# Kernel tuning notes

Hardware: AMD Instinct MI355X
Metric: run time of the kernel (lower is better)

The kernel has to match this reference:

```python
import jax, jax.numpy as jnp
import numpy as np

N_USERS = 50000
N_ITEMS = 50000
N_NODES = N_USERS + N_ITEMS   # 100000
EMB_DIM = 128
N_LAYERS = 3
N_EDGES = 600000


def _segment_softmax(logits, seg, num_segments):
    # numerically-stable softmax over edges grouped by segment id
    m = jax.ops.segment_max(logits, seg, num_segments=num_segments)
    e = jnp.exp(logits - m[seg])
    s = jax.ops.segment_sum(e, seg, num_segments=num_segments)
    return e / s[seg]


def setup_inputs() -> dict:
    key = jax.random.key(0)
    k1, k2, k3, k4 = jax.random.split(key, 4)
    embedding = jax.random.normal(k1, (N_NODES, EMB_DIM), jnp.float32) * 0.1  # init std=0.1
    src = jax.random.randint(k2, (N_EDGES,), 0, N_NODES, dtype=jnp.int32)
    tgt = jax.random.randint(k3, (N_EDGES,), 0, N_NODES, dtype=jnp.int32)
    edge_index = jnp.stack([src, tgt], axis=0)  # [2, E]
    edge_attrs = jax.random.normal(k4, (N_EDGES,), jnp.float32)
    return {"embedding": embedding, "edge_index": edge_index, "edge_attrs": edge_attrs}


def reference(embedding, edge_index, edge_attrs):
    from_, to_ = edge_index[0], edge_index[1]
    # DySimGCF edge normalization: sqrt(incoming_softmax * outgoing_softmax)
    incoming = _segment_softmax(edge_attrs, to_, N_NODES)
    outgoing = _segment_softmax(edge_attrs, from_, N_NODES)
    norm = jnp.sqrt(incoming * outgoing)  # [E]

    emb0 = embedding
    embs = [emb0]
    emb = emb0
    for _ in range(N_LAYERS):
        # gather source embeddings, scale, scatter-add into targets
        msgs = norm[:, None] * emb[from_]                         # [E, D]
        emb = jax.ops.segment_sum(msgs, to_, num_segments=N_NODES)  # [N, D]
        embs.append(emb)
    out = jnp.mean(jnp.stack(embs, axis=0), axis=0)  # layer-averaged embeddings
    return (emb0, out)
```

## Files before the change

### kernel.cpp

```cpp
#include <hip/hip_runtime.h>
#include <math.h>

#define N_NODES 100000
#define EMB_DIM 128
#define N_EDGES 600000
#define SCAN_BLOCKS ((N_NODES + 255) / 256)

__global__ void k_init(float* __restrict__ sum_out, int* __restrict__ deg) {
    int i = blockIdx.x * blockDim.x + threadIdx.x;
    if (i < N_NODES) {
        sum_out[i] = 0.0f;
        deg[i]     = 0;
    }
}

__global__ void k_edge(const int* __restrict__ from_, const int* __restrict__ to_,
                       const float* __restrict__ attr,
                       float* __restrict__ sum_out, int* __restrict__ deg) {
    int e = blockIdx.x * blockDim.x + threadIdx.x;
    if (e >= N_EDGES) return;
    atomicAdd(&sum_out[from_[e]], expf(attr[e]));
    atomicAdd(&deg[to_[e]], 1);
}

__global__ void k_scan1(const int* __restrict__ deg, int* __restrict__ local,
                        int* __restrict__ blockSums) {
    __shared__ int tmp[256];
    int t = threadIdx.x;
    int i = blockIdx.x * 256 + t;
    int v = (i < N_NODES) ? deg[i] : 0;
    tmp[t] = v;
    __syncthreads();
    for (int ofs = 1; ofs < 256; ofs <<= 1) {
        int add = (t >= ofs) ? tmp[t - ofs] : 0;
        __syncthreads();
        tmp[t] += add;
        __syncthreads();
    }
    if (i < N_NODES) local[i] = tmp[t] - v;
    if (t == 255) blockSums[blockIdx.x] = tmp[255];
}

__global__ void k_scan2(int* __restrict__ blockSums) {
    __shared__ int tmp[256];
    int t = threadIdx.x;
    int i0 = t * 2, i1 = t * 2 + 1;
    int a = (i0 < SCAN_BLOCKS) ? blockSums[i0] : 0;
    int b = (i1 < SCAN_BLOCKS) ? blockSums[i1] : 0;
    int s = a + b;
    tmp[t] = s;
    __syncthreads();
    for (int ofs = 1; ofs < 256; ofs <<= 1) {
        int add = (t >= ofs) ? tmp[t - ofs] : 0;
        __syncthreads();
        tmp[t] += add;
        __syncthreads();
    }
    int pre = tmp[t] - s;
    if (i0 < SCAN_BLOCKS) blockSums[i0] = pre;
    if (i1 < SCAN_BLOCKS) blockSums[i1] = pre + a;
}

__global__ void k_scan3(const int* __restrict__ local, const int* __restrict__ blockSums,
                        int* __restrict__ row_ptr, int* __restrict__ cursor) {
    int i = blockIdx.x * 256 + threadIdx.x;
    if (i < N_NODES) {
        int r = local[i] + blockSums[blockIdx.x];
        row_ptr[i] = r;
        cursor[i]  = r;
    }
    if (i == 0) row_ptr[N_NODES] = N_EDGES;
}

__global__ void k_fill(const int* __restrict__ from_, const int* __restrict__ to_,
                       const float* __restrict__ attr,
                       int* __restrict__ cursor, int* __restrict__ col,
                       float* __restrict__ val) {
    int e = blockIdx.x * blockDim.x + threadIdx.x;
    if (e >= N_EDGES) return;
    int t = to_[e];
    int pos = atomicAdd(&cursor[t], 1);
    col[pos] = from_[e];
    val[pos] = expf(attr[e]);
}

__global__ void k_norm(const int* __restrict__ row_ptr, const int* __restrict__ col,
                       const float* __restrict__ sum_out, float* __restrict__ val) {
    int r = blockIdx.x * 256 + threadIdx.x;
    if (r >= N_NODES) return;
    int beg = row_ptr[r], end = row_ptr[r + 1];
    float s = 0.0f;
    for (int e = beg; e < end; ++e) s += val[e];
    for (int e = beg; e < end; ++e) {
        val[e] = val[e] * rsqrtf(s * sum_out[col[e]]);
    }
}

template<int MODE>
__launch_bounds__(256)
__global__ void k_spmm(const int* __restrict__ row_ptr, const int* __restrict__ col,
                       const float* __restrict__ val,
                       const float* __restrict__ src, float* __restrict__ dst,
                       float* __restrict__ acc, const float* __restrict__ emb0) {
    int gid = blockIdx.x * 256 + threadIdx.x;
    int row = gid >> 4;
    if (row >= N_NODES) return;
    int lane = threadIdx.x & 15;
    int beg = row_ptr[row], end = row_ptr[row + 1];
    int d0 = lane * 4;
    float4 s0 = make_float4(0.f, 0.f, 0.f, 0.f);
    float4 s1 = make_float4(0.f, 0.f, 0.f, 0.f);
    int e = beg;
    for (; e + 2 <= end; e += 2) {
        int   c0 = col[e],   c1 = col[e + 1];
        float v0 = val[e],   v1 = val[e + 1];
        const float* b0 = src + (size_t)c0 * EMB_DIM + d0;
        const float* b1 = src + (size_t)c1 * EMB_DIM + d0;
        float4 x0 = *reinterpret_cast<const float4*>(b0);
        float4 x1 = *reinterpret_cast<const float4*>(b0 + 64);
        float4 y0 = *reinterpret_cast<const float4*>(b1);
        float4 y1 = *reinterpret_cast<const float4*>(b1 + 64);
        s0.x = fmaf(v0, x0.x, s0.x); s0.y = fmaf(v0, x0.y, s0.y);
        s0.z = fmaf(v0, x0.z, s0.z); s0.w = fmaf(v0, x0.w, s0.w);
        s1.x = fmaf(v0, x1.x, s1.x); s1.y = fmaf(v0, x1.y, s1.y);
        s1.z = fmaf(v0, x1.z, s1.z); s1.w = fmaf(v0, x1.w, s1.w);
        s0.x = fmaf(v1, y0.x, s0.x); s0.y = fmaf(v1, y0.y, s0.y);
        s0.z = fmaf(v1, y0.z, s0.z); s0.w = fmaf(v1, y0.w, s0.w);
        s1.x = fmaf(v1, y1.x, s1.x); s1.y = fmaf(v1, y1.y, s1.y);
        s1.z = fmaf(v1, y1.z, s1.z); s1.w = fmaf(v1, y1.w, s1.w);
    }
    if (e < end) {
        int   c = col[e];
        float v = val[e];
        const float* base = src + (size_t)c * EMB_DIM + d0;
        float4 x0 = *reinterpret_cast<const float4*>(base);
        float4 x1 = *reinterpret_cast<const float4*>(base + 64);
        s0.x = fmaf(v, x0.x, s0.x); s0.y = fmaf(v, x0.y, s0.y);
        s0.z = fmaf(v, x0.z, s0.z); s0.w = fmaf(v, x0.w, s0.w);
        s1.x = fmaf(v, x1.x, s1.x); s1.y = fmaf(v, x1.y, s1.y);
        s1.z = fmaf(v, x1.z, s1.z); s1.w = fmaf(v, x1.w, s1.w);
    }
    size_t o = (size_t)row * EMB_DIM + d0;
    if (MODE != 2) {
        *reinterpret_cast<float4*>(dst + o)      = s0;
        *reinterpret_cast<float4*>(dst + o + 64) = s1;
    }
    float4 a0, a1;
    if (MODE == 0) {
        float4 z0 = *reinterpret_cast<const float4*>(emb0 + o);
        float4 z1 = *reinterpret_cast<const float4*>(emb0 + o + 64);
        a0.x = z0.x + s0.x; a0.y = z0.y + s0.y; a0.z = z0.z + s0.z; a0.w = z0.w + s0.w;
        a1.x = z1.x + s1.x; a1.y = z1.y + s1.y; a1.z = z1.z + s1.z; a1.w = z1.w + s1.w;
    } else {
        a0 = *reinterpret_cast<float4*>(acc + o);
        a1 = *reinterpret_cast<float4*>(acc + o + 64);
        a0.x += s0.x; a0.y += s0.y; a0.z += s0.z; a0.w += s0.w;
        a1.x += s1.x; a1.y += s1.y; a1.z += s1.z; a1.w += s1.w;
        if (MODE == 2) {
            a0.x *= 0.25f; a0.y *= 0.25f; a0.z *= 0.25f; a0.w *= 0.25f;
            a1.x *= 0.25f; a1.y *= 0.25f; a1.z *= 0.25f; a1.w *= 0.25f;
        }
    }
    *reinterpret_cast<float4*>(acc + o)      = a0;
    *reinterpret_cast<float4*>(acc + o + 64) = a1;
}

extern "C" void kernel_launch(void* const* d_in, const int* in_sizes, int n_in,
                              void* d_out, int out_size, void* d_ws, size_t ws_size,
                              hipStream_t stream) {
    const float* embedding  = (const float*)d_in[0];
    const int*   edge_index = (const int*)d_in[1];
    const float* edge_attrs = (const float*)d_in[2];
    const int* from_ = edge_index;
    const int* to_   = edge_index + N_EDGES;

    float* out_emb0 = (float*)d_out;
    float* acc      = (float*)d_out + (size_t)N_NODES * EMB_DIM;
    float* buf1     = out_emb0;

    char* ws = (char*)d_ws;
    size_t off = 0;
    auto alloc = [&](size_t bytes) -> void* {
        void* p = ws + off;
        off += (bytes + 255) & ~(size_t)255;
        return p;
    };
    float* buf0    = (float*)alloc(sizeof(float) * (size_t)N_NODES * EMB_DIM);
    float* sum_out = (float*)alloc(sizeof(float) * N_NODES);
    int*   deg     = (int*)  alloc(sizeof(int)   * N_NODES);
    int*   scanloc = (int*)  alloc(sizeof(int)   * N_NODES);
    int*   bsums   = (int*)  alloc(sizeof(int)   * SCAN_BLOCKS);
    int*   row_ptr = (int*)  alloc(sizeof(int)   * (N_NODES + 1));
    int*   cursor  = (int*)  alloc(sizeof(int)   * N_NODES);
    int*   col     = (int*)  alloc(sizeof(int)   * N_EDGES);
    float* val     = (float*)alloc(sizeof(float) * N_EDGES);

    const int nblk = SCAN_BLOCKS;
    const int eblk = (N_EDGES + 255) / 256;
    const int sblk = (N_NODES * 16 + 255) / 256;

    k_init<<<nblk, 256, 0, stream>>>(sum_out, deg);
    k_edge<<<eblk, 256, 0, stream>>>(from_, to_, edge_attrs, sum_out, deg);
    k_scan1<<<nblk, 256, 0, stream>>>(deg, scanloc, bsums);
    k_scan2<<<1, 256, 0, stream>>>(bsums);
    k_scan3<<<nblk, 256, 0, stream>>>(scanloc, bsums, row_ptr, cursor);
    k_fill<<<eblk, 256, 0, stream>>>(from_, to_, edge_attrs, cursor, col, val);
    k_norm<<<nblk, 256, 0, stream>>>(row_ptr, col, sum_out, val);

    k_spmm<0><<<sblk, 256, 0, stream>>>(row_ptr, col, val, embedding, buf0, acc, embedding);
    k_spmm<1><<<sblk, 256, 0, stream>>>(row_ptr, col, val, buf0, buf1, acc, embedding);
    k_spmm<2><<<sblk, 256, 0, stream>>>(row_ptr, col, val, buf1, buf0, acc, embedding);

    hipMemcpyAsync(out_emb0, embedding, sizeof(float) * (size_t)N_NODES * EMB_DIM,
                   hipMemcpyDeviceToDevice, stream);
}
```

Baseline: 425.2 us.

## Store intermediate layer embeddings in bf16 and fuse final layer averaging

Converts the input embedding to packed bf16 and keeps the intermediate layer outputs in bf16, which halves the bytes read by each gather-heavy SpMM. The final layer kernel now computes the layer mean in one place from emb0, the two bf16 intermediates and its own result, and it also writes the emb0 copy, so the running accumulator and the separate memcpy are gone. The edge loop is unrolled to 4 edges. The trade-off is bf16 rounding error accumulating across layers, which may break a tight tolerance.

```diff
diff --git a/kernel.cpp b/kernel.cpp
--- a/kernel.cpp
+++ b/kernel.cpp
@@ -1,10 +1,16 @@
 #include <hip/hip_runtime.h>
 #include <math.h>
+#include <stdint.h>
 
 #define N_NODES 100000
 #define EMB_DIM 128
 #define N_EDGES 600000
 #define SCAN_BLOCKS ((N_NODES + 255) / 256)
+
+__device__ __forceinline__ unsigned int f2b(float f) {
+    unsigned int b = __float_as_uint(f);
+    return (b + 0x7FFFu + ((b >> 16) & 1u)) >> 16;
+}
 
 __global__ void k_init(float* __restrict__ sum_out, int* __restrict__ deg) {
     int i = blockIdx.x * blockDim.x + threadIdx.x;
@@ -96,73 +102,90 @@
     }
 }
 
-template<int MODE>
+__global__ void k_cvt(const float* __restrict__ in, uint4* __restrict__ out) {
+    int i = blockIdx.x * 256 + threadIdx.x;
+    const int total = N_NODES * EMB_DIM / 8;
+    if (i >= total) return;
+    const float4* p = reinterpret_cast<const float4*>(in) + (size_t)i * 2;
+    float4 a = p[0], b = p[1];
+    uint4 q;
+    q.x = f2b(a.x) | (f2b(a.y) << 16);
+    q.y = f2b(a.z) | (f2b(a.w) << 16);
+    q.z = f2b(b.x) | (f2b(b.y) << 16);
+    q.w = f2b(b.z) | (f2b(b.w) << 16);
+    out[i] = q;
+}
+
+#define UNPACK_FMA(q, v)                                      \
+    s0 = fmaf(v, __uint_as_float((q).x << 16), s0);           \
+    s1 = fmaf(v, __uint_as_float((q).x & 0xFFFF0000u), s1);   \
+    s2 = fmaf(v, __uint_as_float((q).y << 16), s2);           \
+    s3 = fmaf(v, __uint_as_float((q).y & 0xFFFF0000u), s3);   \
+    s4 = fmaf(v, __uint_as_float((q).z << 16), s4);           \
+    s5 = fmaf(v, __uint_as_float((q).z & 0xFFFF0000u), s5);   \
+    s6 = fmaf(v, __uint_as_float((q).w << 16), s6);           \
+    s7 = fmaf(v, __uint_as_float((q).w & 0xFFFF0000u), s7);
+
+template<int FINAL>
 __launch_bounds__(256)
 __global__ void k_spmm(const int* __restrict__ row_ptr, const int* __restrict__ col,
                        const float* __restrict__ val,
-                       const float* __restrict__ src, float* __restrict__ dst,
-                       float* __restrict__ acc, const float* __restrict__ emb0) {
+                       const uint4* __restrict__ srcb, uint4* __restrict__ dstb,
+                       const float* __restrict__ emb0,
+                       const uint4* __restrict__ e1b, const uint4* __restrict__ e2b,
+                       float* __restrict__ out_acc, float* __restrict__ out_emb0) {
     int gid = blockIdx.x * 256 + threadIdx.x;
     int row = gid >> 4;
     if (row >= N_NODES) return;
     int lane = threadIdx.x & 15;
     int beg = row_ptr[row], end = row_ptr[row + 1];
-    int d0 = lane * 4;
-    float4 s0 = make_float4(0.f, 0.f, 0.f, 0.f);
-    float4 s1 = make_float4(0.f, 0.f, 0.f, 0.f);
+    float s0 = 0.f, s1 = 0.f, s2 = 0.f, s3 = 0.f, s4 = 0.f, s5 = 0.f, s6 = 0.f, s7 = 0.f;
     int e = beg;
-    for (; e + 2 <= end; e += 2) {
-        int   c0 = col[e],   c1 = col[e + 1];
-        float v0 = val[e],   v1 = val[e + 1];
-        const float* b0 = src + (size_t)c0 * EMB_DIM + d0;
-        const float* b1 = src + (size_t)c1 * EMB_DIM + d0;
-        float4 x0 = *reinterpret_cast<const float4*>(b0);
-        float4 x1 = *reinterpret_cast<const float4*>(b0 + 64);
-        float4 y0 = *reinterpret_cast<const float4*>(b1);
-        float4 y1 = *reinterpret_cast<const float4*>(b1 + 64);
-        s0.x = fmaf(v0, x0.x, s0.x); s0.y = fmaf(v0, x0.y, s0.y);
-        s0.z = fmaf(v0, x0.z, s0.z); s0.w = fmaf(v0, x0.w, s0.w);
-        s1.x = fmaf(v0, x1.x, s1.x); s1.y = fmaf(v0, x1.y, s1.y);
-        s1.z = fmaf(v0, x1.z, s1.z); s1.w = fmaf(v0, x1.w, s1.w);
-        s0.x = fmaf(v1, y0.x, s0.x); s0.y = fmaf(v1, y0.y, s0.y);
-        s0.z = fmaf(v1, y0.z, s0.z); s0.w = fmaf(v1, y0.w, s0.w);
-        s1.x = fmaf(v1, y1.x, s1.x); s1.y = fmaf(v1, y1.y, s1.y);
-        s1.z = fmaf(v1, y1.z, s1.z); s1.w = fmaf(v1, y1.w, s1.w);
-    }
-    if (e < end) {
+    for (; e + 4 <= end; e += 4) {
+        int   c0 = col[e], c1 = col[e + 1], c2 = col[e + 2], c3 = col[e + 3];
+        float v0 = val[e], v1 = val[e + 1], v2 = val[e + 2], v3 = val[e + 3];
+        uint4 qa = srcb[(size_t)c0 * 16 + lane];
+        uint4 qb = srcb[(size_t)c1 * 16 + lane];
+        uint4 qc = srcb[(size_t)c2 * 16 + lane];
+        uint4 qd = srcb[(size_t)c3 * 16 + lane];
+        UNPACK_FMA(qa, v0)
+        UNPACK_FMA(qb, v1)
+        UNPACK_FMA(qc, v2)
+        UNPACK_FMA(qd, v3)
+    }
+    for (; e < end; ++e) {
         int   c = col[e];
         float v = val[e];
-        const float* base = src + (size_t)c * EMB_DIM + d0;
-        float4 x0 = *reinterpret_cast<const float4*>(base);
-        float4 x1 = *reinterpret_cast<const float4*>(base + 64);
-        s0.x = fmaf(v, x0.x, s0.x); s0.y = fmaf(v, x0.y, s0.y);
-        s0.z = fmaf(v, x0.z, s0.z); s0.w = fmaf(v, x0.w, s0.w);
-        s1.x = fmaf(v, x1.x, s1.x); s1.y = fmaf(v, x1.y, s1.y);
-        s1.z = fmaf(v, x1.z, s1.z); s1.w = fmaf(v, x1.w, s1.w);
-    }
-    size_t o = (size_t)row * EMB_DIM + d0;
-    if (MODE != 2) {
-        *reinterpret_cast<float4*>(dst + o)      = s0;
-        *reinterpret_cast<float4*>(dst + o + 64) = s1;
-    }
-    float4 a0, a1;
-    if (MODE == 0) {
-        float4 z0 = *reinterpret_cast<const float4*>(emb0 + o);
-        float4 z1 = *reinterpret_cast<const float4*>(emb0 + o + 64);
-        a0.x = z0.x + s0.x; a0.y = z0.y + s0.y; a0.z = z0.z + s0.z; a0.w = z0.w + s0.w;
-        a1.x = z1.x + s1.x; a1.y = z1.y + s1.y; a1.z = z1.z + s1.z; a1.w = z1.w + s1.w;
+        uint4 q = srcb[(size_t)c * 16 + lane];
+        UNPACK_FMA(q, v)
+    }
+    if (!FINAL) {
+        uint4 q;
+        q.x = f2b(s0) | (f2b(s1) << 16);
+        q.y = f2b(s2) | (f2b(s3) << 16);
+        q.z = f2b(s4) | (f2b(s5) << 16);
+        q.w = f2b(s6) | (f2b(s7) << 16);
+        dstb[(size_t)row * 16 + lane] = q;
     } else {
-        a0 = *reinterpret_cast<float4*>(acc + o);
-        a1 = *reinterpret_cast<float4*>(acc + o + 64);
-        a0.x += s0.x; a0.y += s0.y; a0.z += s0.z; a0.w += s0.w;
-        a1.x += s1.x; a1.y += s1.y; a1.z += s1.z; a1.w += s1.w;
-        if (MODE == 2) {
-            a0.x *= 0.25f; a0.y *= 0.25f; a0.z *= 0.25f; a0.w *= 0.25f;
-            a1.x *= 0.25f; a1.y *= 0.25f; a1.z *= 0.25f; a1.w *= 0.25f;
-        }
-    }
-    *reinterpret_cast<float4*>(acc + o)      = a0;
-    *reinterpret_cast<float4*>(acc + o + 64) = a1;
+        size_t o = (size_t)row * EMB_DIM + lane * 8;
+        float4 a0 = *reinterpret_cast<const float4*>(emb0 + o);
+        float4 a1 = *reinterpret_cast<const float4*>(emb0 + o + 4);
+        *reinterpret_cast<float4*>(out_emb0 + o)     = a0;
+        *reinterpret_cast<float4*>(out_emb0 + o + 4) = a1;
+        uint4 q1 = e1b[(size_t)row * 16 + lane];
+        uint4 q2 = e2b[(size_t)row * 16 + lane];
+        float4 r0, r1;
+        r0.x = (a0.x + __uint_as_float(q1.x << 16)          + __uint_as_float(q2.x << 16)          + s0) * 0.25f;
+        r0.y = (a0.y + __uint_as_float(q1.x & 0xFFFF0000u)  + __uint_as_float(q2.x & 0xFFFF0000u)  + s1) * 0.25f;
+        r0.z = (a0.z + __uint_as_float(q1.y << 16)          + __uint_as_float(q2.y << 16)          + s2) * 0.25f;
+        r0.w = (a0.w + __uint_as_float(q1.y & 0xFFFF0000u)  + __uint_as_float(q2.y & 0xFFFF0000u)  + s3) * 0.25f;
+        r1.x = (a1.x + __uint_as_float(q1.z << 16)          + __uint_as_float(q2.z << 16)          + s4) * 0.25f;
+        r1.y = (a1.y + __uint_as_float(q1.z & 0xFFFF0000u)  + __uint_as_float(q2.z & 0xFFFF0000u)  + s5) * 0.25f;
+        r1.z = (a1.z + __uint_as_float(q1.w << 16)          + __uint_as_float(q2.w << 16)          + s6) * 0.25f;
+        r1.w = (a1.w + __uint_as_float(q1.w & 0xFFFF0000u)  + __uint_as_float(q2.w & 0xFFFF0000u)  + s7) * 0.25f;
+        *reinterpret_cast<float4*>(out_acc + o)     = r0;
+        *reinterpret_cast<float4*>(out_acc + o + 4) = r1;
+    }
 }
 
 extern "C" void kernel_launch(void* const* d_in, const int* in_sizes, int n_in,
@@ -175,8 +198,8 @@
     const int* to_   = edge_index + N_EDGES;
 
     float* out_emb0 = (float*)d_out;
-    float* acc      = (float*)d_out + (size_t)N_NODES * EMB_DIM;
-    float* buf1     = out_emb0;
+    float* out_acc  = (float*)d_out + (size_t)N_NODES * EMB_DIM;
+    uint4* emb0b    = (uint4*)d_out;
 
     char* ws = (char*)d_ws;
     size_t off = 0;
@@ -185,7 +208,8 @@
         off += (bytes + 255) & ~(size_t)255;
         return p;
     };
-    float* buf0    = (float*)alloc(sizeof(float) * (size_t)N_NODES * EMB_DIM);
+    uint4* e1b     = (uint4*)alloc((size_t)N_NODES * 16 * sizeof(uint4));
+    uint4* e2b     = (uint4*)alloc((size_t)N_NODES * 16 * sizeof(uint4));
     float* sum_out = (float*)alloc(sizeof(float) * N_NODES);
     int*   deg     = (int*)  alloc(sizeof(int)   * N_NODES);
     int*   scanloc = (int*)  alloc(sizeof(int)   * N_NODES);
@@ -197,6 +221,7 @@
 
     const int nblk = SCAN_BLOCKS;
     const int eblk = (N_EDGES + 255) / 256;
+    const int cblk = (N_NODES * EMB_DIM / 8 + 255) / 256;
     const int sblk = (N_NODES * 16 + 255) / 256;
 
     k_init<<<nblk, 256, 0, stream>>>(sum_out, deg);
@@ -206,11 +231,12 @@
     k_scan3<<<nblk, 256, 0, stream>>>(scanloc, bsums, row_ptr, cursor);
     k_fill<<<eblk, 256, 0, stream>>>(from_, to_, edge_attrs, cursor, col, val);
     k_norm<<<nblk, 256, 0, stream>>>(row_ptr, col, sum_out, val);
-
-    k_spmm<0><<<sblk, 256, 0, stream>>>(row_ptr, col, val, embedding, buf0, acc, embedding);
-    k_spmm<1><<<sblk, 256, 0, stream>>>(row_ptr, col, val, buf0, buf1, acc, embedding);
-    k_spmm<2><<<sblk, 256, 0, stream>>>(row_ptr, col, val, buf1, buf0, acc, embedding);
-
-    hipMemcpyAsync(out_emb0, embedding, sizeof(float) * (size_t)N_NODES * EMB_DIM,
-                   hipMemcpyDeviceToDevice, stream);
-}
+    k_cvt<<<cblk, 256, 0, stream>>>(embedding, emb0b);
+
+    k_spmm<0><<<sblk, 256, 0, stream>>>(row_ptr, col, val, emb0b, e1b,
+                                        nullptr, nullptr, nullptr, nullptr, nullptr);
+    k_spmm<0><<<sblk, 256, 0, stream>>>(row_ptr, col, val, e1b, e2b,
+                                        nullptr, nullptr, nullptr, nullptr, nullptr);
+    k_spmm<1><<<sblk, 256, 0, stream>>>(row_ptr, col, val, e2b, nullptr,
+                                        embedding, e1b, e2b, out_acc, out_emb0);
+}
```

New measurement: 348.1 us. 18.1% less time.
